# Kernel optimization log

Hardware: AMD Instinct MI355X
Metric: run time of the kernel (lower is better)

The kernel has to match this reference:

```python
import jax, jax.numpy as jnp
import numpy as np

SOS, EOS, PAD = 1, 2, 0


def setup_inputs() -> dict:
    key = jax.random.key(0)
    ks = jax.random.split(key, 8)
    n, d_z, d_h, d_emb, V = 8192, 128, 512, 128, 64
    s = lambda k, shape, scale: jax.random.normal(k, shape, jnp.float32) * scale
    return {
        "Z": jax.random.normal(ks[0], (n, d_z), jnp.float32),
        "emb": s(ks[1], (V, d_emb), 0.1),
        "z2h_w": s(ks[2], (d_h, d_z), 0.05),
        "z2h_b": jnp.zeros((d_h,), jnp.float32),
        "w_ih0": s(ks[3], (3 * d_h, d_emb), 0.05),
        "w_ih_rest": s(ks[4], (2, 3 * d_h, d_h), 0.05),
        "w_hh": s(ks[5], (3, 3 * d_h, d_h), 0.05),
        "b_ih": jnp.zeros((3, 3 * d_h), jnp.float32),
        "b_hh": jnp.zeros((3, 3 * d_h), jnp.float32),
        "h2v_w": s(ks[6], (V, d_h), 0.05),
        "h2v_b": jnp.zeros((V,), jnp.float32),
        "max_len": 80,
    }


def _gru_cell(x, h, w_ih, w_hh, b_ih, b_hh):
    # torch GRU gate order: r, z, n
    gi = x @ w_ih.T + b_ih
    gh = h @ w_hh.T + b_hh
    i_r, i_z, i_n = jnp.split(gi, 3, axis=-1)
    h_r, h_z, h_n = jnp.split(gh, 3, axis=-1)
    r = jax.nn.sigmoid(i_r + h_r)
    z = jax.nn.sigmoid(i_z + h_z)
    g = jnp.tanh(i_n + r * h_n)
    return (1.0 - z) * g + z * h


def _decode(Z, emb, z2h_w, z2h_b, w_ih0, w_ih_rest, w_hh, b_ih, b_hh, h2v_w, h2v_b, max_len):
    n = Z.shape[0]
    L = w_hh.shape[0]
    h0 = Z @ z2h_w.T + z2h_b                      # [n, d_h], repeated over layers
    H = jnp.broadcast_to(h0[None], (L,) + h0.shape)
    x0 = jnp.full((n,), SOS, jnp.int32)
    eos0 = jnp.zeros((n,), bool)
    w_ih = [w_ih0] + [w_ih_rest[i] for i in range(w_ih_rest.shape[0])]

    def step(carry, t):
        H, x_prev, eos = carry
        inp = emb[x_prev]                          # [n, d_emb]
        Hs = []
        for l in range(L):                         # small fixed layer loop
            h_new = _gru_cell(inp, H[l], w_ih[l], w_hh[l], b_ih[l], b_hh[l])
            Hs.append(h_new)
            inp = h_new
        probs = jax.nn.softmax(inp @ h2v_w.T + h2v_b, axis=-1)  # [n, V]
        x_t = jnp.argmax(probs, axis=-1).astype(jnp.int32)      # ModeSampler
        tok = jnp.where(eos, PAD, x_t)             # masked write into X_gen
        new_eos = (~eos) & (x_t == EOS)
        return (jnp.stack(Hs), x_t, eos | new_eos), (tok, new_eos, probs)

    ts = jnp.arange(1, max_len, dtype=jnp.int32)
    _, (toks, new_eos, probs) = jax.lax.scan(step, (H, x0, eos0), ts)
    X_gen = jnp.concatenate([jnp.full((n, 1), SOS, jnp.int32), toks.T], axis=1)  # [n, max_len]
    any_eos = new_eos.any(axis=0)
    first_t = ts[jnp.argmax(new_eos, axis=0)]
    seq_lens = jnp.where(any_eos, first_t + 1, max_len).astype(jnp.int32)
    return X_gen, seq_lens, probs


def reference(Z, emb, z2h_w, z2h_b, w_ih0, w_ih_rest, w_hh, b_ih, b_hh, h2v_w, h2v_b, max_len):
    X_gen, seq_lens, _ = _decode(Z, emb, z2h_w, z2h_b, w_ih0, w_ih_rest,
                                 w_hh, b_ih, b_hh, h2v_w, h2v_b, max_len)
    # torch returns a ragged list X_gen[i, :seq_lens[i]]; we return the padded
    # tensor plus lengths (jit-compatible equivalent).
    return X_gen, seq_lens
```

## Files before the change

### kernel.cpp

```cpp
#include <hip/hip_runtime.h>
#include <math.h>

#define NSEQ 8192
#define DH 512
#define DZ 128
#define DE 128
#define VOCAB 64
#define TMAX 80
#define SOS 1
#define EOS_TOK 2

#define TMR 64
#define TNCOL 32

typedef _Float16 half_t;
typedef half_t h8 __attribute__((ext_vector_type(8)));
typedef float f4 __attribute__((ext_vector_type(4)));

__device__ __forceinline__ float sigf(float x) { return 1.0f / (1.0f + expf(-x)); }

__device__ __forceinline__ void split2(float v, half_t& hi, half_t& lo) {
    float hf = (float)(half_t)v;
    if (fabsf(v) < 6.2e-5f) hf = 0.0f;
    hi = (half_t)hf;
    lo = (half_t)((v - hf) * 2048.0f);
}

__device__ __forceinline__ float rec2(half_t h, half_t l) {
    return (float)h + (float)l * (1.0f / 2048.0f);
}

__device__ __forceinline__ void gl_lds16(const void* g, void* l) {
    __builtin_amdgcn_global_load_lds((const __attribute__((address_space(1))) void*)g,
                                     (__attribute__((address_space(3))) void*)l, 16, 0, 0);
}

__device__ __forceinline__ void swizzle_rc(int bid, int& r, int& c) {
    const int x = bid & 7;
    const int q = bid >> 3;
    r = (q & 15) * 8 + x;
    c = q >> 4;
}

__global__ __launch_bounds__(256) void init_kernel(int* __restrict__ x_prev,
                                                   int* __restrict__ eos,
                                                   int* __restrict__ out,
                                                   int* __restrict__ list,
                                                   int* __restrict__ count) {
    int i = blockIdx.x * 256 + threadIdx.x;
    x_prev[i] = SOS;
    eos[i] = 0;
    list[i] = i;
    out[i * TMAX] = SOS;
    out[NSEQ * TMAX + i] = TMAX;
    if (i == 0) count[0] = NSEQ;
}

__global__ __launch_bounds__(1024) void compact_kernel(const int* __restrict__ eos,
                                                       int* __restrict__ list,
                                                       int* __restrict__ count) {
    __shared__ int part[1024];
    __shared__ int slist[NSEQ];
    const int tid = threadIdx.x;
    const int base = tid * 8;
    int f[8], s = 0;
#pragma unroll
    for (int i = 0; i < 8; ++i) { f[i] = eos[base + i] ? 0 : 1; s += f[i]; }
    part[tid] = s;
    __syncthreads();
    for (int off = 1; off < 1024; off <<= 1) {
        int v = (tid >= off) ? part[tid - off] : 0;
        __syncthreads();
        part[tid] += v;
        __syncthreads();
    }
    const int total = part[1023];
    int p = part[tid] - s;
#pragma unroll
    for (int i = 0; i < 8; ++i) if (f[i]) slist[p++] = base + i;
    __syncthreads();
    if (tid == 0) {
        count[0] = total;
        if (total > 0) {
            const int last = slist[total - 1];
            const int padn = (total + 63) & ~63;
            for (int k = total; k < padn; ++k) slist[k] = last;
        }
    }
    __syncthreads();
    const int padn = (total + 63) & ~63;
    for (int k = tid; k < padn; k += 1024) list[k] = slist[k];
}

__global__ __launch_bounds__(256) void h0_kernel(const float* __restrict__ Z,
                                                 const float* __restrict__ w,
                                                 const float* __restrict__ b,
                                                 half_t* __restrict__ B0h, half_t* __restrict__ B0l,
                                                 half_t* __restrict__ B1h, half_t* __restrict__ B1l,
                                                 half_t* __restrict__ B2h, half_t* __restrict__ B2l) {
    __shared__ float zrow[DZ];
    const int i = blockIdx.x;
    const int tid = threadIdx.x;
    if (tid < DZ) zrow[tid] = Z[(size_t)i * DZ + tid];
    __syncthreads();
    for (int j = tid; j < DH; j += 256) {
        double s = (double)b[j];
        const float* wr = w + (size_t)j * DZ;
#pragma unroll 8
        for (int k = 0; k < DZ; ++k) s += (double)zrow[k] * (double)wr[k];
        float sf = (float)s;
        half_t hi, lo;
        split2(sf, hi, lo);
        size_t o = (size_t)i * DH + j;
        B0h[o] = hi; B0l[o] = lo;
        B1h[o] = hi; B1l[o] = lo;
        B2h[o] = hi; B2l[o] = lo;
    }
}

__global__ __launch_bounds__(256) void gi0_kernel(const float* __restrict__ emb,
                                                  const float* __restrict__ w_ih0,
                                                  const float* __restrict__ b_ih0,
                                                  double* __restrict__ tab) {
    __shared__ float e[DE];
    const int x = blockIdx.x;
    const int tid = threadIdx.x;
    if (tid < DE) e[tid] = emb[(size_t)x * DE + tid];
    __syncthreads();
    for (int j = tid; j < 3 * DH; j += 256) {
        double s = (double)b_ih0[j];
        const float* wr = w_ih0 + (size_t)j * DE;
#pragma unroll 8
        for (int k = 0; k < DE; ++k) s += (double)e[k] * (double)wr[k];
        tab[(size_t)x * 3 * DH + j] = s;
    }
}

__global__ __launch_bounds__(256) void wsplit_kernel(const float* __restrict__ w,
                                                     half_t* __restrict__ hi,
                                                     half_t* __restrict__ lo, int n) {
    int i = blockIdx.x * 256 + threadIdx.x;
    if (i < n) {
        half_t h, l;
        split2(w[i], h, l);
        hi[i] = h; lo[i] = l;
    }
}


__global__ __launch_bounds__(256, 3) void layer0_mfma(
    const half_t* __restrict__ Hch, const half_t* __restrict__ Hcl,
    half_t* __restrict__ Hnh, half_t* __restrict__ Hnl,
    const half_t* __restrict__ Wh, const half_t* __restrict__ Wl,
    const float* __restrict__ b_hh0,
    const double* __restrict__ tab,
    const int* __restrict__ x_prev,
    const int* __restrict__ list, const int* __restrict__ count) {
    int rt, ct;
    swizzle_rc(blockIdx.x, rt, ct);
    const int row0 = rt * TMR;
    const int cnt = count[0];
    if (row0 >= cnt) return;
    const int col0 = ct * TNCOL;

    __shared__ char sm[40960];
    const int tid = threadIdx.x;
    const int lane = tid & 63, w = tid >> 6;
    const int lr = lane & 15, lq = lane >> 4;
    const int wr0 = (w >> 1) * 32, wc0 = (w & 1) * 16;

    int aoff[2], boff[3];
#pragma unroll
    for (int i = 0; i < 2; ++i) {
        int u = i * 256 + tid, r = u >> 3, s = u & 7;
        aoff[i] = list[row0 + r] * 1024 + ((s ^ (r & 7)) << 4);
    }
#pragma unroll
    for (int j = 0; j < 3; ++j) {
        int u = j * 256 + tid, br = u >> 3, s = u & 7;
        int wr = (br >> 5) * DH + col0 + (br & 31);
        boff[j] = wr * 1024 + ((s ^ (br & 7)) << 4);
    }

    int fa[2][2], fb[3][2];
#pragma unroll
    for (int rf = 0; rf < 2; ++rf)
#pragma unroll
        for (int ks = 0; ks < 2; ++ks) {
            int row = wr0 + rf * 16 + lr;
            int sb = ks * 4 + lq;
            fa[rf][ks] = row * 128 + ((sb ^ (row & 7)) << 4);
        }
#pragma unroll
    for (int g = 0; g < 3; ++g)
#pragma unroll
        for (int ks = 0; ks < 2; ++ks) {
            int br = g * 32 + wc0 + lr;
            int sb = ks * 4 + lq;
            fb[g][ks] = br * 128 + ((sb ^ (br & 7)) << 4);
        }

    f4 hh[2][3] = {}, cc[2][3] = {};
    const char* Ah = (const char*)Hch;
    const char* Al = (const char*)Hcl;
    const char* Bh = (const char*)Wh;
    const char* Bl = (const char*)Wl;

    for (int kc = 0; kc < 8; ++kc) {
        const int kb = kc * 128;
#pragma unroll
        for (int i = 0; i < 2; ++i) {
            gl_lds16(Ah + aoff[i] + kb, sm + (i * 256 + tid) * 16);
            gl_lds16(Al + aoff[i] + kb, sm + 8192 + (i * 256 + tid) * 16);
        }
#pragma unroll
        for (int j = 0; j < 3; ++j) {
            gl_lds16(Bh + boff[j] + kb, sm + 16384 + (j * 256 + tid) * 16);
            gl_lds16(Bl + boff[j] + kb, sm + 28672 + (j * 256 + tid) * 16);
        }
        __syncthreads();
#pragma unroll
        for (int ks = 0; ks < 2; ++ks) {
            h8 a0h = *(const h8*)(sm + fa[0][ks]);
            h8 a0l = *(const h8*)(sm + 8192 + fa[0][ks]);
            h8 a1h = *(const h8*)(sm + fa[1][ks]);
            h8 a1l = *(const h8*)(sm + 8192 + fa[1][ks]);
#pragma unroll
            for (int g = 0; g < 3; ++g) {
                h8 bh = *(const h8*)(sm + 16384 + fb[g][ks]);
                h8 bl = *(const h8*)(sm + 28672 + fb[g][ks]);
                hh[0][g] = __builtin_amdgcn_mfma_f32_16x16x32_f16(a0h, bh, hh[0][g], 0, 0, 0);
                cc[0][g] = __builtin_amdgcn_mfma_f32_16x16x32_f16(a0h, bl, cc[0][g], 0, 0, 0);
                cc[0][g] = __builtin_amdgcn_mfma_f32_16x16x32_f16(a0l, bh, cc[0][g], 0, 0, 0);
                hh[1][g] = __builtin_amdgcn_mfma_f32_16x16x32_f16(a1h, bh, hh[1][g], 0, 0, 0);
                cc[1][g] = __builtin_amdgcn_mfma_f32_16x16x32_f16(a1h, bl, cc[1][g], 0, 0, 0);
                cc[1][g] = __builtin_amdgcn_mfma_f32_16x16x32_f16(a1l, bh, cc[1][g], 0, 0, 0);
            }
        }
        __syncthreads();
    }

    const float inv = 1.0f / 2048.0f;
#pragma unroll
    for (int rf = 0; rf < 2; ++rf) {
        f4 pR = hh[rf][0] + cc[rf][0] * inv;
        f4 pZ = hh[rf][1] + cc[rf][1] * inv;
        f4 pN = hh[rf][2] + cc[rf][2] * inv;
        const int gj = col0 + wc0 + lr;
#pragma unroll
        for (int reg = 0; reg < 4; ++reg) {
            const int rl = wr0 + rf * 16 + lq * 4 + reg;
            const int gi = list[row0 + rl];
            const double* tr = tab + (size_t)x_prev[gi] * (3 * DH);
            float xr = (float)(tr[gj] + (double)pR[reg] + (double)b_hh0[gj]);
            float xz = (float)(tr[DH + gj] + (double)pZ[reg] + (double)b_hh0[DH + gj]);
            float hn_pre = pN[reg] + b_hh0[2 * DH + gj];
            float r = sigf(xr), z = sigf(xz);
            float g = tanhf((float)(tr[2 * DH + gj] + (double)r * (double)hn_pre));
            size_t o = (size_t)gi * DH + gj;
            float ho = rec2(Hch[o], Hcl[o]);
            float h = (1.0f - z) * g + z * ho;
            half_t oh, ol;
            split2(h, oh, ol);
            Hnh[o] = oh; Hnl[o] = ol;
        }
    }
}

__global__ __launch_bounds__(256, 3) void layer12_mfma(
    const half_t* __restrict__ Xh, const half_t* __restrict__ Xl,
    const half_t* __restrict__ Hch, const half_t* __restrict__ Hcl,
    half_t* __restrict__ Hnh, half_t* __restrict__ Hnl,
    const half_t* __restrict__ Wih_h, const half_t* __restrict__ Wih_l,
    const half_t* __restrict__ Whh_h, const half_t* __restrict__ Whh_l,
    const float* __restrict__ b_ih, const float* __restrict__ b_hh,
    const int* __restrict__ list, const int* __restrict__ count) {
    int rt, ct;
    swizzle_rc(blockIdx.x, rt, ct);
    const int row0 = rt * TMR;
    const int cnt = count[0];
    if (row0 >= cnt) return;
    const int col0 = ct * TNCOL;

    __shared__ char sm[40960];
    const int tid = threadIdx.x;
    const int lane = tid & 63, w = tid >> 6;
    const int lr = lane & 15, lq = lane >> 4;
    const int wr0 = (w >> 1) * 32, wc0 = (w & 1) * 16;

    int aoff[2], boff[3];
#pragma unroll
    for (int i = 0; i < 2; ++i) {
        int u = i * 256 + tid, r = u >> 3, s = u & 7;
        aoff[i] = list[row0 + r] * 1024 + ((s ^ (r & 7)) << 4);
    }
#pragma unroll
    for (int j = 0; j < 3; ++j) {
        int u = j * 256 + tid, br = u >> 3, s = u & 7;
        int wr = (br >> 5) * DH + col0 + (br & 31);
        boff[j] = wr * 1024 + ((s ^ (br & 7)) << 4);
    }

    int fa[2][2], fb[3][2];
#pragma unroll
    for (int rf = 0; rf < 2; ++rf)
#pragma unroll
        for (int ks = 0; ks < 2; ++ks) {
            int row = wr0 + rf * 16 + lr;
            int sb = ks * 4 + lq;
            fa[rf][ks] = row * 128 + ((sb ^ (row & 7)) << 4);
        }
#pragma unroll
    for (int g = 0; g < 3; ++g)
#pragma unroll
        for (int ks = 0; ks < 2; ++ks) {
            int br = g * 32 + wc0 + lr;
            int sb = ks * 4 + lq;
            fb[g][ks] = br * 128 + ((sb ^ (br & 7)) << 4);
        }

    f4 hh[2][3] = {}, cc[2][3] = {}, niS[2] = {};

    for (int kc = 0; kc < 16; ++kc) {
        const int kb = (kc & 7) * 128;
        const char* As_h = (kc < 8) ? (const char*)Xh : (const char*)Hch;
        const char* As_l = (kc < 8) ? (const char*)Xl : (const char*)Hcl;
        const char* Ws_h = (kc < 8) ? (const char*)Wih_h : (const char*)Whh_h;
        const char* Ws_l = (kc < 8) ? (const char*)Wih_l : (const char*)Whh_l;
#pragma unroll
        for (int i = 0; i < 2; ++i) {
            gl_lds16(As_h + aoff[i] + kb, sm + (i * 256 + tid) * 16);
            gl_lds16(As_l + aoff[i] + kb, sm + 8192 + (i * 256 + tid) * 16);
        }
#pragma unroll
        for (int j = 0; j < 3; ++j) {
            gl_lds16(Ws_h + boff[j] + kb, sm + 16384 + (j * 256 + tid) * 16);
            gl_lds16(Ws_l + boff[j] + kb, sm + 28672 + (j * 256 + tid) * 16);
        }
        __syncthreads();
#pragma unroll
        for (int ks = 0; ks < 2; ++ks) {
            h8 a0h = *(const h8*)(sm + fa[0][ks]);
            h8 a0l = *(const h8*)(sm + 8192 + fa[0][ks]);
            h8 a1h = *(const h8*)(sm + fa[1][ks]);
            h8 a1l = *(const h8*)(sm + 8192 + fa[1][ks]);
#pragma unroll
            for (int g = 0; g < 3; ++g) {
                h8 bh = *(const h8*)(sm + 16384 + fb[g][ks]);
                h8 bl = *(const h8*)(sm + 28672 + fb[g][ks]);
                hh[0][g] = __builtin_amdgcn_mfma_f32_16x16x32_f16(a0h, bh, hh[0][g], 0, 0, 0);
                cc[0][g] = __builtin_amdgcn_mfma_f32_16x16x32_f16(a0h, bl, cc[0][g], 0, 0, 0);
                cc[0][g] = __builtin_amdgcn_mfma_f32_16x16x32_f16(a0l, bh, cc[0][g], 0, 0, 0);
                hh[1][g] = __builtin_amdgcn_mfma_f32_16x16x32_f16(a1h, bh, hh[1][g], 0, 0, 0);
                cc[1][g] = __builtin_amdgcn_mfma_f32_16x16x32_f16(a1h, bl, cc[1][g], 0, 0, 0);
                cc[1][g] = __builtin_amdgcn_mfma_f32_16x16x32_f16(a1l, bh, cc[1][g], 0, 0, 0);
            }
        }
        __syncthreads();
        if (kc == 7) {
#pragma unroll
            for (int rf = 0; rf < 2; ++rf) {
                niS[rf] = hh[rf][2] + cc[rf][2] * (1.0f / 2048.0f);
                f4 zz = {0.0f, 0.0f, 0.0f, 0.0f};
                hh[rf][2] = zz;
                cc[rf][2] = zz;
            }
        }
    }

    const float inv = 1.0f / 2048.0f;
#pragma unroll
    for (int rf = 0; rf < 2; ++rf) {
        f4 pR = hh[rf][0] + cc[rf][0] * inv;
        f4 pZ = hh[rf][1] + cc[rf][1] * inv;
        f4 pNH = hh[rf][2] + cc[rf][2] * inv;
        f4 pNI = niS[rf];
        const int gj = col0 + wc0 + lr;
#pragma unroll
        for (int reg = 0; reg < 4; ++reg) {
            const int rl = wr0 + rf * 16 + lq * 4 + reg;
            const int gi = list[row0 + rl];
            float xr = pR[reg] + b_ih[gj] + b_hh[gj];
            float xz = pZ[reg] + b_ih[DH + gj] + b_hh[DH + gj];
            float xi = pNI[reg] + b_ih[2 * DH + gj];
            float hn_pre = pNH[reg] + b_hh[2 * DH + gj];
            float r = sigf(xr), z = sigf(xz);
            float g = tanhf(xi + r * hn_pre);
            size_t o = (size_t)gi * DH + gj;
            float ho = rec2(Hch[o], Hcl[o]);
            float h = (1.0f - z) * g + z * ho;
            half_t oh, ol;
            split2(h, oh, ol);
            Hnh[o] = oh; Hnl[o] = ol;
        }
    }
}

__global__ __launch_bounds__(256) void logits_kernel(const half_t* __restrict__ H2h,
                                                     const half_t* __restrict__ H2l,
                                                     const float* __restrict__ h2v_w,
                                                     const float* __restrict__ h2v_b,
                                                     int* __restrict__ x_prev,
                                                     int* __restrict__ eos,
                                                     int* __restrict__ out,
                                                     const int* __restrict__ list,
                                                     const int* __restrict__ count,
                                                     int t) {
    const int rowbase = blockIdx.x * 16;
    const int cnt = count[0];
    if (rowbase >= cnt) return;

    __shared__ float Ws[VOCAB][65];
    __shared__ float Hs[16][65];
    const int tid = threadIdx.x;
    double acc[4] = {0.0, 0.0, 0.0, 0.0};

    for (int k0 = 0; k0 < DH; k0 += 64) {
        __syncthreads();
#pragma unroll
        for (int it = 0; it < 16; ++it) {
            int idx = tid + 256 * it;
            int v = idx >> 6, k = idx & 63;
            Ws[v][k] = h2v_w[(size_t)v * DH + k0 + k];
        }
#pragma unroll
        for (int it = 0; it < 4; ++it) {
            int idx = tid + 256 * it;
            int r = idx >> 6, k = idx & 63;
            size_t o = (size_t)list[rowbase + r] * DH + k0 + k;
            Hs[r][k] = rec2(H2h[o], H2l[o]);
        }
        __syncthreads();
        const int r = tid >> 4;
        const int vb = (tid & 15) * 4;
#pragma unroll 16
        for (int k = 0; k < 64; ++k) {
            double h = (double)Hs[r][k];
            acc[0] += h * (double)Ws[vb + 0][k];
            acc[1] += h * (double)Ws[vb + 1][k];
            acc[2] += h * (double)Ws[vb + 2][k];
            acc[3] += h * (double)Ws[vb + 3][k];
        }
    }

    const int r = tid >> 4;
    const int vb = (tid & 15) * 4;
    float lf[4];
#pragma unroll
    for (int vv = 0; vv < 4; ++vv) lf[vv] = (float)(acc[vv] + (double)h2v_b[vb + vv]);

    float m = fmaxf(fmaxf(lf[0], lf[1]), fmaxf(lf[2], lf[3]));
#pragma unroll
    for (int off = 1; off < 16; off <<= 1) m = fmaxf(m, __shfl_xor(m, off));
    float e[4];
    float ssum = 0.f;
#pragma unroll
    for (int vv = 0; vv < 4; ++vv) { e[vv] = expf(lf[vv] - m); ssum += e[vv]; }
#pragma unroll
    for (int off = 1; off < 16; off <<= 1) ssum += __shfl_xor(ssum, off);

    float best = e[0] / ssum;
    int bi = vb;
#pragma unroll
    for (int vv = 1; vv < 4; ++vv) {
        float pv = e[vv] / ssum;
        if (pv > best) { best = pv; bi = vb + vv; }
    }
#pragma unroll
    for (int off = 1; off < 16; off <<= 1) {
        float ov = __shfl_xor(best, off);
        int oi = __shfl_xor(bi, off);
        if (ov > best || (ov == best && oi < bi)) { best = ov; bi = oi; }
    }
    if ((tid & 15) == 0) {
        const int gi = list[rowbase + r];
        const int ee = eos[gi];
        const int xt = bi;
        out[(size_t)gi * TMAX + t] = ee ? 0 : xt;
        if (!ee && xt == EOS_TOK) {
            out[NSEQ * TMAX + gi] = t + 1;
            eos[gi] = 1;
        }
        x_prev[gi] = xt;
    }
}

extern "C" void kernel_launch(void* const* d_in, const int* in_sizes, int n_in,
                              void* d_out, int out_size, void* d_ws, size_t ws_size,
                              hipStream_t stream) {
    const float* Z        = (const float*)d_in[0];
    const float* emb      = (const float*)d_in[1];
    const float* z2h_w    = (const float*)d_in[2];
    const float* z2h_b    = (const float*)d_in[3];
    const float* w_ih0    = (const float*)d_in[4];
    const float* w_ih_rest= (const float*)d_in[5];
    const float* w_hh     = (const float*)d_in[6];
    const float* b_ih     = (const float*)d_in[7];
    const float* b_hh     = (const float*)d_in[8];
    const float* h2v_w    = (const float*)d_in[9];
    const float* h2v_b    = (const float*)d_in[10];

    int* out = (int*)d_out;
    char* p = (char*)d_ws;
    const size_t HS = (size_t)NSEQ * DH * sizeof(half_t);
    half_t* Bh[4]; half_t* Bl[4];
    for (int i = 0; i < 4; ++i) { Bh[i] = (half_t*)p; p += HS; }
    for (int i = 0; i < 4; ++i) { Bl[i] = (half_t*)p; p += HS; }
    double* tab = (double*)p; p += (size_t)VOCAB * 3 * DH * sizeof(double);
    const size_t WH = (size_t)3 * DH * DH;
    half_t* wih_h = (half_t*)p; p += 2 * WH * sizeof(half_t);
    half_t* wih_l = (half_t*)p; p += 2 * WH * sizeof(half_t);
    half_t* whh_h = (half_t*)p; p += 3 * WH * sizeof(half_t);
    half_t* whh_l = (half_t*)p; p += 3 * WH * sizeof(half_t);
    int* x_prev = (int*)p; p += NSEQ * sizeof(int);
    int* eos    = (int*)p; p += NSEQ * sizeof(int);
    int* alist  = (int*)p; p += NSEQ * sizeof(int);
    int* acount = (int*)p; p += 256;

    hipMemsetAsync(out, 0, (size_t)NSEQ * TMAX * sizeof(int), stream);
    init_kernel<<<NSEQ / 256, 256, 0, stream>>>(x_prev, eos, out, alist, acount);
    h0_kernel<<<NSEQ, 256, 0, stream>>>(Z, z2h_w, z2h_b,
                                        Bh[0], Bl[0], Bh[1], Bl[1], Bh[2], Bl[2]);
    gi0_kernel<<<VOCAB, 256, 0, stream>>>(emb, w_ih0, b_ih, tab);
    wsplit_kernel<<<(int)((2 * WH + 255) / 256), 256, 0, stream>>>(w_ih_rest, wih_h, wih_l, (int)(2 * WH));
    wsplit_kernel<<<(int)((3 * WH + 255) / 256), 256, 0, stream>>>(w_hh, whh_h, whh_l, (int)(3 * WH));

    int c0 = 0, c1 = 1, c2 = 2, sp = 3;
    const int lgrid = (NSEQ / TMR) * (DH / TNCOL);
    for (int t = 1; t < TMAX; ++t) {
        layer0_mfma<<<lgrid, 256, 0, stream>>>(Bh[c0], Bl[c0], Bh[sp], Bl[sp],
            whh_h, whh_l, b_hh, tab, x_prev, alist, acount);
        layer12_mfma<<<lgrid, 256, 0, stream>>>(Bh[sp], Bl[sp], Bh[c1], Bl[c1], Bh[c0], Bl[c0],
            wih_h, wih_l, whh_h + WH, whh_l + WH, b_ih + 3 * DH, b_hh + 3 * DH, alist, acount);
        layer12_mfma<<<lgrid, 256, 0, stream>>>(Bh[c0], Bl[c0], Bh[c2], Bl[c2], Bh[c1], Bl[c1],
            wih_h + WH, wih_l + WH, whh_h + 2 * WH, whh_l + 2 * WH,
            b_ih + 6 * DH, b_hh + 6 * DH, alist, acount);
        logits_kernel<<<NSEQ / 16, 256, 0, stream>>>(Bh[c1], Bl[c1], h2v_w, h2v_b,
                                                     x_prev, eos, out, alist, acount, t);
        if (t < TMAX - 1)
            compact_kernel<<<1, 1024, 0, stream>>>(eos, alist, acount);
        int n0 = sp, n1 = c0, n2 = c1, nsp = c2;
        c0 = n0; c1 = n1; c2 = n2; sp = nsp;
    }
}
```

Baseline: 14.98 ms.

## Enlarge GRU GEMM tiles to 128x64 with 32x32 MFMA and double-buffered LDS

The GRU layer kernels move from 64x32 tiles on 256 threads to 128x64 tiles on 512 threads, and switch from 16x16x32 to 32x32x16 MFMA. The K loop now uses a 64-byte step with double-buffered LDS staging through global_load_lds, using explicit vmcnt waits, s_barrier and setprio. This is meant to raise operand reuse per loaded byte, halve block-level syncs, and overlap loads with math. The costs are more LDS per block, padding the active list to 128 rows (wasted rows for small counts), and the LDS XOR swizzle is gone, which may bring bank conflicts.

Result: slower. 19.64 ms (+31.1%).

```diff
diff --git a/kernel.cpp b/kernel.cpp
--- a/kernel.cpp
+++ b/kernel.cpp
@@ -10,12 +10,11 @@
 #define SOS 1
 #define EOS_TOK 2
 
-#define TMR 64
-#define TNCOL 32
+#define TMR 128
 
 typedef _Float16 half_t;
 typedef half_t h8 __attribute__((ext_vector_type(8)));
-typedef float f4 __attribute__((ext_vector_type(4)));
+typedef float f16v __attribute__((ext_vector_type(16)));
 
 __device__ __forceinline__ float sigf(float x) { return 1.0f / (1.0f + expf(-x)); }
 
@@ -35,11 +34,11 @@
                                      (__attribute__((address_space(3))) void*)l, 16, 0, 0);
 }
 
-__device__ __forceinline__ void swizzle_rc(int bid, int& r, int& c) {
+__device__ __forceinline__ void swz(int bid, int& r, int& c) {
     const int x = bid & 7;
     const int q = bid >> 3;
-    r = (q & 15) * 8 + x;
-    c = q >> 4;
+    r = (q & 7) * 8 + x;
+    c = q >> 3;
 }
 
 __global__ __launch_bounds__(256) void init_kernel(int* __restrict__ x_prev,
@@ -83,12 +82,12 @@
         count[0] = total;
         if (total > 0) {
             const int last = slist[total - 1];
-            const int padn = (total + 63) & ~63;
+            const int padn = (total + 127) & ~127;
             for (int k = total; k < padn; ++k) slist[k] = last;
         }
     }
     __syncthreads();
-    const int padn = (total + 63) & ~63;
+    const int padn = (total + 127) & ~127;
     for (int k = tid; k < padn; k += 1024) list[k] = slist[k];
 }
 
@@ -148,7 +147,7 @@
 }
 
 
-__global__ __launch_bounds__(256, 3) void layer0_mfma(
+__global__ __launch_bounds__(512, 2) void layer0_mfma(
     const half_t* __restrict__ Hch, const half_t* __restrict__ Hcl,
     half_t* __restrict__ Hnh, half_t* __restrict__ Hnl,
     const half_t* __restrict__ Wh, const half_t* __restrict__ Wl,
@@ -157,117 +156,109 @@
     const int* __restrict__ x_prev,
     const int* __restrict__ list, const int* __restrict__ count) {
     int rt, ct;
-    swizzle_rc(blockIdx.x, rt, ct);
+    swz(blockIdx.x, rt, ct);
     const int row0 = rt * TMR;
     const int cnt = count[0];
     if (row0 >= cnt) return;
-    const int col0 = ct * TNCOL;
-
-    __shared__ char sm[40960];
+
+    __shared__ __align__(16) char sm[81920];
     const int tid = threadIdx.x;
-    const int lane = tid & 63, w = tid >> 6;
-    const int lr = lane & 15, lq = lane >> 4;
-    const int wr0 = (w >> 1) * 32, wc0 = (w & 1) * 16;
-
-    int aoff[2], boff[3];
-#pragma unroll
-    for (int i = 0; i < 2; ++i) {
-        int u = i * 256 + tid, r = u >> 3, s = u & 7;
-        aoff[i] = list[row0 + r] * 1024 + ((s ^ (r & 7)) << 4);
-    }
-#pragma unroll
-    for (int j = 0; j < 3; ++j) {
-        int u = j * 256 + tid, br = u >> 3, s = u & 7;
-        int wr = (br >> 5) * DH + col0 + (br & 31);
-        boff[j] = wr * 1024 + ((s ^ (br & 7)) << 4);
-    }
-
-    int fa[2][2], fb[3][2];
-#pragma unroll
-    for (int rf = 0; rf < 2; ++rf)
+    const int w = tid >> 6, l = tid & 63;
+    const int l31 = l & 31, lh = l >> 5;
+    const int rw = w >> 1, ch = w & 1;
+
+    const int arow = (tid >> 5) * 8 + (tid & 7);
+    const int kch  = (tid >> 3) & 3;
+    const size_t asrc = (size_t)list[row0 + arow] * 1024 + kch * 16;
+    const int alds = tid * 16;
+    const int b1row = arow;
+    const size_t bsrc1 = (size_t)((b1row >> 6) * DH + ct * 64 + (b1row & 63)) * 1024 + kch * 16;
+    const int blds1 = tid * 16;
+    const int b2row = 128 + arow;
+    const size_t bsrc2 = (size_t)((b2row >> 6) * DH + ct * 64 + (b2row & 63)) * 1024 + kch * 16;
+    const int blds2 = 8192 + tid * 16;
+    const bool havB2 = (tid < 256);
+
+    const int afr = rw * 32 + l31;
+    const int afo = (afr >> 3) * 512 + lh * 128 + (afr & 7) * 16;
+    int bfo[3];
+#pragma unroll
+    for (int g = 0; g < 3; ++g) {
+        const int br = g * 64 + ch * 32 + l31;
+        bfo[g] = (br >> 3) * 512 + lh * 128 + (br & 7) * 16;
+    }
+
+    f16v hh[3] = {}, cc[3] = {};
+
+    auto stage = [&](int bb, int kcb) {
+        const size_t ko = (size_t)kcb * 64;
+        gl_lds16((const char*)Hch + asrc + ko, sm + bb + alds);
+        gl_lds16((const char*)Hcl + asrc + ko, sm + bb + 8192 + alds);
+        gl_lds16((const char*)Wh + bsrc1 + ko, sm + bb + 16384 + blds1);
+        gl_lds16((const char*)Wl + bsrc1 + ko, sm + bb + 28672 + blds1);
+        if (havB2) {
+            gl_lds16((const char*)Wh + bsrc2 + ko, sm + bb + 16384 + blds2);
+            gl_lds16((const char*)Wl + bsrc2 + ko, sm + bb + 28672 + blds2);
+        }
+    };
+
+    stage(0, 0);
+    for (int kc = 0; kc < 16; ++kc) {
+        const int cb = (kc & 1) * 40960;
+        if (kc < 15) {
+            stage(cb ^ 40960, kc + 1);
+            if (havB2) asm volatile("s_waitcnt vmcnt(6)" ::: "memory");
+            else       asm volatile("s_waitcnt vmcnt(4)" ::: "memory");
+        } else {
+            asm volatile("s_waitcnt vmcnt(0)" ::: "memory");
+        }
+        __builtin_amdgcn_s_barrier();
+        __builtin_amdgcn_sched_barrier(0);
+        __builtin_amdgcn_s_setprio(1);
+        const char* bp = sm + cb;
 #pragma unroll
         for (int ks = 0; ks < 2; ++ks) {
-            int row = wr0 + rf * 16 + lr;
-            int sb = ks * 4 + lq;
-            fa[rf][ks] = row * 128 + ((sb ^ (row & 7)) << 4);
-        }
-#pragma unroll
-    for (int g = 0; g < 3; ++g)
-#pragma unroll
-        for (int ks = 0; ks < 2; ++ks) {
-            int br = g * 32 + wc0 + lr;
-            int sb = ks * 4 + lq;
-            fb[g][ks] = br * 128 + ((sb ^ (br & 7)) << 4);
-        }
-
-    f4 hh[2][3] = {}, cc[2][3] = {};
-    const char* Ah = (const char*)Hch;
-    const char* Al = (const char*)Hcl;
-    const char* Bh = (const char*)Wh;
-    const char* Bl = (const char*)Wl;
-
-    for (int kc = 0; kc < 8; ++kc) {
-        const int kb = kc * 128;
-#pragma unroll
-        for (int i = 0; i < 2; ++i) {
-            gl_lds16(Ah + aoff[i] + kb, sm + (i * 256 + tid) * 16);
-            gl_lds16(Al + aoff[i] + kb, sm + 8192 + (i * 256 + tid) * 16);
-        }
-#pragma unroll
-        for (int j = 0; j < 3; ++j) {
-            gl_lds16(Bh + boff[j] + kb, sm + 16384 + (j * 256 + tid) * 16);
-            gl_lds16(Bl + boff[j] + kb, sm + 28672 + (j * 256 + tid) * 16);
-        }
-        __syncthreads();
-#pragma unroll
-        for (int ks = 0; ks < 2; ++ks) {
-            h8 a0h = *(const h8*)(sm + fa[0][ks]);
-            h8 a0l = *(const h8*)(sm + 8192 + fa[0][ks]);
-            h8 a1h = *(const h8*)(sm + fa[1][ks]);
-            h8 a1l = *(const h8*)(sm + 8192 + fa[1][ks]);
+            h8 ah = *(const h8*)(bp + afo + ks * 256);
+            h8 al = *(const h8*)(bp + 8192 + afo + ks * 256);
 #pragma unroll
             for (int g = 0; g < 3; ++g) {
-                h8 bh = *(const h8*)(sm + 16384 + fb[g][ks]);
-                h8 bl = *(const h8*)(sm + 28672 + fb[g][ks]);
-                hh[0][g] = __builtin_amdgcn_mfma_f32_16x16x32_f16(a0h, bh, hh[0][g], 0, 0, 0);
-                cc[0][g] = __builtin_amdgcn_mfma_f32_16x16x32_f16(a0h, bl, cc[0][g], 0, 0, 0);
-                cc[0][g] = __builtin_amdgcn_mfma_f32_16x16x32_f16(a0l, bh, cc[0][g], 0, 0, 0);
-                hh[1][g] = __builtin_amdgcn_mfma_f32_16x16x32_f16(a1h, bh, hh[1][g], 0, 0, 0);
-                cc[1][g] = __builtin_amdgcn_mfma_f32_16x16x32_f16(a1h, bl, cc[1][g], 0, 0, 0);
-                cc[1][g] = __builtin_amdgcn_mfma_f32_16x16x32_f16(a1l, bh, cc[1][g], 0, 0, 0);
+                h8 bh = *(const h8*)(bp + 16384 + bfo[g] + ks * 256);
+                h8 bl = *(const h8*)(bp + 28672 + bfo[g] + ks * 256);
+                hh[g] = __builtin_amdgcn_mfma_f32_32x32x16_f16(ah, bh, hh[g], 0, 0, 0);
+                cc[g] = __builtin_amdgcn_mfma_f32_32x32x16_f16(ah, bl, cc[g], 0, 0, 0);
+                cc[g] = __builtin_amdgcn_mfma_f32_32x32x16_f16(al, bh, cc[g], 0, 0, 0);
             }
         }
-        __syncthreads();
-    }
-
+        __builtin_amdgcn_s_setprio(0);
+        asm volatile("s_waitcnt lgkmcnt(0)" ::: "memory");
+        __builtin_amdgcn_s_barrier();
+    }
+
+    const int colg = ct * 64 + ch * 32 + l31;
     const float inv = 1.0f / 2048.0f;
 #pragma unroll
-    for (int rf = 0; rf < 2; ++rf) {
-        f4 pR = hh[rf][0] + cc[rf][0] * inv;
-        f4 pZ = hh[rf][1] + cc[rf][1] * inv;
-        f4 pN = hh[rf][2] + cc[rf][2] * inv;
-        const int gj = col0 + wc0 + lr;
-#pragma unroll
-        for (int reg = 0; reg < 4; ++reg) {
-            const int rl = wr0 + rf * 16 + lq * 4 + reg;
-            const int gi = list[row0 + rl];
-            const double* tr = tab + (size_t)x_prev[gi] * (3 * DH);
-            float xr = (float)(tr[gj] + (double)pR[reg] + (double)b_hh0[gj]);
-            float xz = (float)(tr[DH + gj] + (double)pZ[reg] + (double)b_hh0[DH + gj]);
-            float hn_pre = pN[reg] + b_hh0[2 * DH + gj];
-            float r = sigf(xr), z = sigf(xz);
-            float g = tanhf((float)(tr[2 * DH + gj] + (double)r * (double)hn_pre));
-            size_t o = (size_t)gi * DH + gj;
-            float ho = rec2(Hch[o], Hcl[o]);
-            float h = (1.0f - z) * g + z * ho;
-            half_t oh, ol;
-            split2(h, oh, ol);
-            Hnh[o] = oh; Hnl[o] = ol;
-        }
-    }
-}
-
-__global__ __launch_bounds__(256, 3) void layer12_mfma(
+    for (int r = 0; r < 16; ++r) {
+        const int la = rw * 32 + (r & 3) + 8 * (r >> 2) + 4 * lh;
+        const int gi = list[row0 + la];
+        const double* tr = tab + (size_t)x_prev[gi] * (3 * DH);
+        float pR = hh[0][r] + cc[0][r] * inv;
+        float pZ = hh[1][r] + cc[1][r] * inv;
+        float pN = hh[2][r] + cc[2][r] * inv;
+        float xr = (float)(tr[colg] + (double)pR + (double)b_hh0[colg]);
+        float xz = (float)(tr[DH + colg] + (double)pZ + (double)b_hh0[DH + colg]);
+        float hn_pre = pN + b_hh0[2 * DH + colg];
+        float rg = sigf(xr), zg = sigf(xz);
+        float gg = tanhf((float)(tr[2 * DH + colg] + (double)rg * (double)hn_pre));
+        size_t o = (size_t)gi * DH + colg;
+        float ho = rec2(Hch[o], Hcl[o]);
+        float hv = (1.0f - zg) * gg + zg * ho;
+        half_t oh, ol;
+        split2(hv, oh, ol);
+        Hnh[o] = oh; Hnl[o] = ol;
+    }
+}
+
+__global__ __launch_bounds__(512, 2) void layer12_mfma(
     const half_t* __restrict__ Xh, const half_t* __restrict__ Xl,
     const half_t* __restrict__ Hch, const half_t* __restrict__ Hcl,
     half_t* __restrict__ Hnh, half_t* __restrict__ Hnl,
@@ -276,123 +267,114 @@
     const float* __restrict__ b_ih, const float* __restrict__ b_hh,
     const int* __restrict__ list, const int* __restrict__ count) {
     int rt, ct;
-    swizzle_rc(blockIdx.x, rt, ct);
+    swz(blockIdx.x, rt, ct);
     const int row0 = rt * TMR;
     const int cnt = count[0];
     if (row0 >= cnt) return;
-    const int col0 = ct * TNCOL;
-
-    __shared__ char sm[40960];
+
+    __shared__ __align__(16) char sm[81920];
     const int tid = threadIdx.x;
-    const int lane = tid & 63, w = tid >> 6;
-    const int lr = lane & 15, lq = lane >> 4;
-    const int wr0 = (w >> 1) * 32, wc0 = (w & 1) * 16;
-
-    int aoff[2], boff[3];
-#pragma unroll
-    for (int i = 0; i < 2; ++i) {
-        int u = i * 256 + tid, r = u >> 3, s = u & 7;
-        aoff[i] = list[row0 + r] * 1024 + ((s ^ (r & 7)) << 4);
-    }
-#pragma unroll
-    for (int j = 0; j < 3; ++j) {
-        int u = j * 256 + tid, br = u >> 3, s = u & 7;
-        int wr = (br >> 5) * DH + col0 + (br & 31);
-        boff[j] = wr * 1024 + ((s ^ (br & 7)) << 4);
-    }
-
-    int fa[2][2], fb[3][2];
-#pragma unroll
-    for (int rf = 0; rf < 2; ++rf)
+    const int w = tid >> 6, l = tid & 63;
+    const int l31 = l & 31, lh = l >> 5;
+    const int rw = w >> 1, ch = w & 1;
+
+    const int arow = (tid >> 5) * 8 + (tid & 7);
+    const int kch  = (tid >> 3) & 3;
+    const size_t asrc = (size_t)list[row0 + arow] * 1024 + kch * 16;
+    const int alds = tid * 16;
+    const int b1row = arow;
+    const size_t bsrc1 = (size_t)((b1row >> 6) * DH + ct * 64 + (b1row & 63)) * 1024 + kch * 16;
+    const int blds1 = tid * 16;
+    const int b2row = 128 + arow;
+    const size_t bsrc2 = (size_t)((b2row >> 6) * DH + ct * 64 + (b2row & 63)) * 1024 + kch * 16;
+    const int blds2 = 8192 + tid * 16;
+    const bool havB2 = (tid < 256);
+
+    const int afr = rw * 32 + l31;
+    const int afo = (afr >> 3) * 512 + lh * 128 + (afr & 7) * 16;
+    int bfo[3];
+#pragma unroll
+    for (int g = 0; g < 3; ++g) {
+        const int br = g * 64 + ch * 32 + l31;
+        bfo[g] = (br >> 3) * 512 + lh * 128 + (br & 7) * 16;
+    }
+
+    f16v hh[3] = {}, cc[3] = {}, niS = {};
+
+    auto stage = [&](int bb, int kcb) {
+        const char* Ah_ = (kcb < 16) ? (const char*)Xh : (const char*)Hch;
+        const char* Al_ = (kcb < 16) ? (const char*)Xl : (const char*)Hcl;
+        const char* Bh_ = (kcb < 16) ? (const char*)Wih_h : (const char*)Whh_h;
+        const char* Bl_ = (kcb < 16) ? (const char*)Wih_l : (const char*)Whh_l;
+        const size_t ko = (size_t)(kcb & 15) * 64;
+        gl_lds16(Ah_ + asrc + ko, sm + bb + alds);
+        gl_lds16(Al_ + asrc + ko, sm + bb + 8192 + alds);
+        gl_lds16(Bh_ + bsrc1 + ko, sm + bb + 16384 + blds1);
+        gl_lds16(Bl_ + bsrc1 + ko, sm + bb + 28672 + blds1);
+        if (havB2) {
+            gl_lds16(Bh_ + bsrc2 + ko, sm + bb + 16384 + blds2);
+            gl_lds16(Bl_ + bsrc2 + ko, sm + bb + 28672 + blds2);
+        }
+    };
+
+    stage(0, 0);
+    for (int kc = 0; kc < 32; ++kc) {
+        const int cb = (kc & 1) * 40960;
+        if (kc < 31) {
+            stage(cb ^ 40960, kc + 1);
+            if (havB2) asm volatile("s_waitcnt vmcnt(6)" ::: "memory");
+            else       asm volatile("s_waitcnt vmcnt(4)" ::: "memory");
+        } else {
+            asm volatile("s_waitcnt vmcnt(0)" ::: "memory");
+        }
+        __builtin_amdgcn_s_barrier();
+        __builtin_amdgcn_sched_barrier(0);
+        __builtin_amdgcn_s_setprio(1);
+        const char* bp = sm + cb;
 #pragma unroll
         for (int ks = 0; ks < 2; ++ks) {
-            int row = wr0 + rf * 16 + lr;
-            int sb = ks * 4 + lq;
-            fa[rf][ks] = row * 128 + ((sb ^ (row & 7)) << 4);
-        }
-#pragma unroll
-    for (int g = 0; g < 3; ++g)
-#pragma unroll
-        for (int ks = 0; ks < 2; ++ks) {
-            int br = g * 32 + wc0 + lr;
-            int sb = ks * 4 + lq;
-            fb[g][ks] = br * 128 + ((sb ^ (br & 7)) << 4);
-        }
-
-    f4 hh[2][3] = {}, cc[2][3] = {}, niS[2] = {};
-
-    for (int kc = 0; kc < 16; ++kc) {
-        const int kb = (kc & 7) * 128;
-        const char* As_h = (kc < 8) ? (const char*)Xh : (const char*)Hch;
-        const char* As_l = (kc < 8) ? (const char*)Xl : (const char*)Hcl;
-        const char* Ws_h = (kc < 8) ? (const char*)Wih_h : (const char*)Whh_h;
-        const char* Ws_l = (kc < 8) ? (const char*)Wih_l : (const char*)Whh_l;
-#pragma unroll
-        for (int i = 0; i < 2; ++i) {
-            gl_lds16(As_h + aoff[i] + kb, sm + (i * 256 + tid) * 16);
-            gl_lds16(As_l + aoff[i] + kb, sm + 8192 + (i * 256 + tid) * 16);
-        }
-#pragma unroll
-        for (int j = 0; j < 3; ++j) {
-            gl_lds16(Ws_h + boff[j] + kb, sm + 16384 + (j * 256 + tid) * 16);
-            gl_lds16(Ws_l + boff[j] + kb, sm + 28672 + (j * 256 + tid) * 16);
-        }
-        __syncthreads();
-#pragma unroll
-        for (int ks = 0; ks < 2; ++ks) {
-            h8 a0h = *(const h8*)(sm + fa[0][ks]);
-            h8 a0l = *(const h8*)(sm + 8192 + fa[0][ks]);
-            h8 a1h = *(const h8*)(sm + fa[1][ks]);
-            h8 a1l = *(const h8*)(sm + 8192 + fa[1][ks]);
+            h8 ah = *(const h8*)(bp + afo + ks * 256);
+            h8 al = *(const h8*)(bp + 8192 + afo + ks * 256);
 #pragma unroll
             for (int g = 0; g < 3; ++g) {
-                h8 bh = *(const h8*)(sm + 16384 + fb[g][ks]);
-                h8 bl = *(const h8*)(sm + 28672 + fb[g][ks]);
-                hh[0][g] = __builtin_amdgcn_mfma_f32_16x16x32_f16(a0h, bh, hh[0][g], 0, 0, 0);
-                cc[0][g] = __builtin_amdgcn_mfma_f32_16x16x32_f16(a0h, bl, cc[0][g], 0, 0, 0);
-                cc[0][g] = __builtin_amdgcn_mfma_f32_16x16x32_f16(a0l, bh, cc[0][g], 0, 0, 0);
-                hh[1][g] = __builtin_amdgcn_mfma_f32_16x16x32_f16(a1h, bh, hh[1][g], 0, 0, 0);
-                cc[1][g] = __builtin_amdgcn_mfma_f32_16x16x32_f16(a1h, bl, cc[1][g], 0, 0, 0);
-                cc[1][g] = __builtin_amdgcn_mfma_f32_16x16x32_f16(a1l, bh, cc[1][g], 0, 0, 0);
+                h8 bh = *(const h8*)(bp + 16384 + bfo[g] + ks * 256);
+                h8 bl = *(const h8*)(bp + 28672 + bfo[g] + ks * 256);
+                hh[g] = __builtin_amdgcn_mfma_f32_32x32x16_f16(ah, bh, hh[g], 0, 0, 0);
+                cc[g] = __builtin_amdgcn_mfma_f32_32x32x16_f16(ah, bl, cc[g], 0, 0, 0);
+                cc[g] = __builtin_amdgcn_mfma_f32_32x32x16_f16(al, bh, cc[g], 0, 0, 0);
             }
         }
-        __syncthreads();
-        if (kc == 7) {
-#pragma unroll
-            for (int rf = 0; rf < 2; ++rf) {
-                niS[rf] = hh[rf][2] + cc[rf][2] * (1.0f / 2048.0f);
-                f4 zz = {0.0f, 0.0f, 0.0f, 0.0f};
-                hh[rf][2] = zz;
-                cc[rf][2] = zz;
-            }
-        }
-    }
-
+        __builtin_amdgcn_s_setprio(0);
+        if (kc == 15) {
+            niS = hh[2] + cc[2] * (1.0f / 2048.0f);
+            f16v zz = {};
+            hh[2] = zz; cc[2] = zz;
+        }
+        asm volatile("s_waitcnt lgkmcnt(0)" ::: "memory");
+        __builtin_amdgcn_s_barrier();
+    }
+
+    const int colg = ct * 64 + ch * 32 + l31;
     const float inv = 1.0f / 2048.0f;
 #pragma unroll
-    for (int rf = 0; rf < 2; ++rf) {
-        f4 pR = hh[rf][0] + cc[rf][0] * inv;
-        f4 pZ = hh[rf][1] + cc[rf][1] * inv;
-        f4 pNH = hh[rf][2] + cc[rf][2] * inv;
-        f4 pNI = niS[rf];
-        const int gj = col0 + wc0 + lr;
-#pragma unroll
-        for (int reg = 0; reg < 4; ++reg) {
-            const int rl = wr0 + rf * 16 + lq * 4 + reg;
-            const int gi = list[row0 + rl];
-            float xr = pR[reg] + b_ih[gj] + b_hh[gj];
-            float xz = pZ[reg] + b_ih[DH + gj] + b_hh[DH + gj];
-            float xi = pNI[reg] + b_ih[2 * DH + gj];
-            float hn_pre = pNH[reg] + b_hh[2 * DH + gj];
-            float r = sigf(xr), z = sigf(xz);
-            float g = tanhf(xi + r * hn_pre);
-            size_t o = (size_t)gi * DH + gj;
-            float ho = rec2(Hch[o], Hcl[o]);
-            float h = (1.0f - z) * g + z * ho;
-            half_t oh, ol;
-            split2(h, oh, ol);
-            Hnh[o] = oh; Hnl[o] = ol;
-        }
+    for (int r = 0; r < 16; ++r) {
+        const int la = rw * 32 + (r & 3) + 8 * (r >> 2) + 4 * lh;
+        const int gi = list[row0 + la];
+        float pR = hh[0][r] + cc[0][r] * inv;
+        float pZ = hh[1][r] + cc[1][r] * inv;
+        float pNH = hh[2][r] + cc[2][r] * inv;
+        float xr = pR + b_ih[colg] + b_hh[colg];
+        float xz = pZ + b_ih[DH + colg] + b_hh[DH + colg];
+        float xi = niS[r] + b_ih[2 * DH + colg];
+        float hn_pre = pNH + b_hh[2 * DH + colg];
+        float rg = sigf(xr), zg = sigf(xz);
+        float gg = tanhf(xi + rg * hn_pre);
+        size_t o = (size_t)gi * DH + colg;
+        float ho = rec2(Hch[o], Hcl[o]);
+        float hv = (1.0f - zg) * gg + zg * ho;
+        half_t oh, ol;
+        split2(hv, oh, ol);
+        Hnh[o] = oh; Hnl[o] = ol;
     }
 }
 
@@ -526,13 +508,13 @@
     wsplit_kernel<<<(int)((3 * WH + 255) / 256), 256, 0, stream>>>(w_hh, whh_h, whh_l, (int)(3 * WH));
 
     int c0 = 0, c1 = 1, c2 = 2, sp = 3;
-    const int lgrid = (NSEQ / TMR) * (DH / TNCOL);
+    const int lgrid = (NSEQ / TMR) * (DH / 64);
     for (int t = 1; t < TMAX; ++t) {
-        layer0_mfma<<<lgrid, 256, 0, stream>>>(Bh[c0], Bl[c0], Bh[sp], Bl[sp],
+        layer0_mfma<<<lgrid, 512, 0, stream>>>(Bh[c0], Bl[c0], Bh[sp], Bl[sp],
             whh_h, whh_l, b_hh, tab, x_prev, alist, acount);
-        layer12_mfma<<<lgrid, 256, 0, stream>>>(Bh[sp], Bl[sp], Bh[c1], Bl[c1], Bh[c0], Bl[c0],
+        layer12_mfma<<<lgrid, 512, 0, stream>>>(Bh[sp], Bl[sp], Bh[c1], Bl[c1], Bh[c0], Bl[c0],
             wih_h, wih_l, whh_h + WH, whh_l + WH, b_ih + 3 * DH, b_hh + 3 * DH, alist, acount);
-        layer12_mfma<<<lgrid, 256, 0, stream>>>(Bh[c0], Bl[c0], Bh[c2], Bl[c2], Bh[c1], Bl[c1],
+        layer12_mfma<<<lgrid, 512, 0, stream>>>(Bh[c0], Bl[c0], Bh[c2], Bl[c2], Bh[c1], Bl[c1],
             wih_h + WH, wih_l + WH, whh_h + 2 * WH, whh_l + 2 * WH,
             b_ih + 6 * DH, b_hh + 6 * DH, alist, acount);
         logits_kernel<<<NSEQ / 16, 256, 0, stream>>>(Bh[c1], Bl[c1], h2v_w, h2v_b,
```
